# Performance work log

Hardware: AMD Instinct MI355X
Metric: run time of the kernel (lower is better)

Reference implementation:

```python
import jax, jax.numpy as jnp
import numpy as np

B, H = 1, 512
NVAR, NCLS = 16384, 65536
NP, NM = 4096, 4096
NEG = -1e30


def setup_inputs() -> dict:
    key = jax.random.key(0)
    ks = jax.random.split(key, 16)
    s = 0.02  # weight init scale
    return {
        "literal_emb": jax.random.normal(ks[0], (B, 2 * NVAR, H), jnp.float32),
        "clause_emb": jax.random.normal(ks[1], (B, NCLS, H), jnp.float32),
        "pos_idx": jax.random.randint(ks[2], (NP,), 0, NCLS),
        "neg_idx": jax.random.randint(ks[3], (NM,), 0, NCLS),
        "keep_mask": jax.random.randint(ks[4], (NP, NM), 0, 2).astype(bool),
        "taken_mask": jax.random.uniform(ks[5], (NP, NM)) < 0.01,  # sparse exclusion set
        "var_K_w": s * jax.random.normal(ks[6], (H, H), jnp.float32),
        "var_K_b": jnp.zeros((H,), jnp.float32),
        "var_Q_w": s * jax.random.normal(ks[7], (H, H), jnp.float32),
        "var_Q_b": jnp.zeros((H,), jnp.float32),
        "var_attn_w": s * jax.random.normal(ks[8], (1, H), jnp.float32),
        "var_attn_b": jnp.zeros((1,), jnp.float32),
        "W_Q_w": s * jax.random.normal(ks[9], (H, H), jnp.float32),
        "W_Q_b": jnp.zeros((H,), jnp.float32),
        "W_K_w": s * jax.random.normal(ks[10], (H, H), jnp.float32),
        "W_K_b": jnp.zeros((H,), jnp.float32),
    }


def reference(literal_emb, clause_emb, pos_idx, neg_idx, keep_mask, taken_mask,
              var_K_w, var_K_b, var_Q_w, var_Q_b, var_attn_w, var_attn_b,
              W_Q_w, W_Q_b, W_K_w, W_K_b):
    n_vars = literal_emb.shape[1] // 2
    # --- select_var: additive attention over positive literals ---
    K = literal_emb[:, :n_vars]                       # [B, V, H]
    K_t = K @ var_K_w.T + var_K_b                     # [B, V, H]
    Q = clause_emb.sum(axis=1)                        # [B, H] (C_aggr='sum')
    Q_t = Q @ var_Q_w.T + var_Q_b                     # [B, H]
    u = (jnp.tanh(K_t + Q_t[:, None, :]) @ var_attn_w.T + var_attn_b)[..., 0]  # [B, V]
    log_score = jax.nn.log_softmax(u, axis=-1)
    var_logp = jnp.max(log_score, axis=-1)            # [B]
    var_idx = jnp.argmax(log_score, axis=-1)          # [B]
    # --- clause-pair attention over pivot pos/neg clause pools ---
    q = clause_emb[:, pos_idx] @ W_Q_w.T + W_Q_b      # [B, NP, H]
    k = clause_emb[:, neg_idx] @ W_K_w.T + W_K_b      # [B, NM, H]
    h = q.shape[-1]
    scores = jnp.einsum('bnh,bmh->bnm', q, k) / jnp.sqrt(jnp.float32(h))
    # mask_grid_asym: drop invalid (keep_mask==0) and already-taken pairs, log-normalize
    valid = keep_mask & (~taken_mask)                 # [NP, NM]
    masked = jnp.where(valid[None], scores, jnp.float32(NEG))
    flat = masked.reshape(masked.shape[0], -1)        # [B, NP*NM]
    logp = jax.nn.log_softmax(flat, axis=-1)
    C_logp = jnp.max(logp, axis=-1)                   # [B]
    C_flat = jnp.argmax(logp, axis=-1)                # [B]
    M = scores.shape[-1]
    ci, cj = C_flat // M, C_flat % M
    c_idx_pos = pos_idx[ci]                           # map back to global clause ids
    c_idx_neg = neg_idx[cj]
    c_logp = C_logp + var_logp                        # [B]
    return (c_logp, c_idx_pos, c_idx_neg, var_idx)
```

## Files before the change

### kernel.cpp

```cpp
#include <hip/hip_runtime.h>
#include <hip/hip_bf16.h>
#include <math.h>

#define HH 512
#define NVARS 16384
#define NPOS 4096
#define NMS 4096
#define NEGV -1.0e30f
#define RSQRT_H 0.04419417382415922f

typedef unsigned short u16;
typedef __attribute__((ext_vector_type(8))) short bf16x8;
typedef __attribute__((ext_vector_type(4))) float f32x4;

struct SPart { float m; float s; int a; int pad; };

__device__ inline u16 f2bf(float f) {
  unsigned u = __float_as_uint(f);
  unsigned r = (u + 0x7fffu + ((u >> 16) & 1u)) >> 16;
  return (u16)r;
}
__device__ inline float bf2f(u16 h) { return __uint_as_float(((unsigned)h) << 16); }

__device__ inline void wreduce_maxidx(float& v, int& idx) {
#pragma unroll
  for (int m = 1; m < 64; m <<= 1) {
    float ov = __shfl_xor(v, m, 64);
    int oi = __shfl_xor(idx, m, 64);
    if (ov > v || (ov == v && oi < idx)) { v = ov; idx = oi; }
  }
}

__device__ inline float wreduce_sum(float v) {
#pragma unroll
  for (int m = 1; m < 64; m <<= 1) v += __shfl_xor(v, m, 64);
  return v;
}

__device__ __forceinline__ void stage_frag(const u16* src, u16* dst) {
  __builtin_amdgcn_global_load_lds(
      (const __attribute__((address_space(1))) void*)src,
      (__attribute__((address_space(3))) void*)dst, 16, 0, 0);
}

__device__ __forceinline__ void do_tofrag(
    const float* __restrict__ src, u16* __restrict__ hi, u16* __restrict__ lo,
    int frag, int lane) {
  const int R = frag >> 4, K = frag & 15;
  const float* p = src + (size_t)(R * 16 + (lane & 15)) * HH + K * 32 + (lane >> 4) * 8;
  float v[8];
  *(float4*)&v[0] = *(const float4*)p;
  *(float4*)&v[4] = *(const float4*)(p + 4);
  u16 h[8], l[8];
#pragma unroll
  for (int e = 0; e < 8; ++e) { h[e] = f2bf(v[e]); l[e] = f2bf(v[e] - bf2f(h[e])); }
  size_t base = (size_t)frag * 512 + (size_t)lane * 8;
  *(ushort4*)(hi + base) = *(ushort4*)&h[0];
  *(ushort4*)(hi + base + 4) = *(ushort4*)&h[4];
  *(ushort4*)(lo + base) = *(ushort4*)&l[0];
  *(ushort4*)(lo + base + 4) = *(ushort4*)&l[4];
}

__global__ __launch_bounds__(256) void wtofrag_kernel(
    const float* __restrict__ varKw, u16* __restrict__ wkhi, u16* __restrict__ wklo,
    const float* __restrict__ WQw, u16* __restrict__ pwqhi, u16* __restrict__ pwqlo,
    const float* __restrict__ WKw, u16* __restrict__ pwkhi, u16* __restrict__ pwklo) {
  const int wb = blockIdx.x;
  const int m = wb >> 7;
  const int frag = (wb & 127) * 4 + (threadIdx.x >> 6);
  const float* src = (m == 0) ? varKw : (m == 1) ? WQw : WKw;
  u16* hi = (m == 0) ? wkhi : (m == 1) ? pwqhi : pwkhi;
  u16* lo = (m == 0) ? wklo : (m == 1) ? pwqlo : pwklo;
  do_tofrag(src, hi, lo, frag, threadIdx.x & 63);
}

__global__ __launch_bounds__(256) void stream_kernel(
    const float* __restrict__ clause, double* __restrict__ qpart,
    const float* __restrict__ lit, u16* __restrict__ lithi, u16* __restrict__ litlo,
    const void* __restrict__ keep, const void* __restrict__ taken,
    unsigned long long* __restrict__ vmask) {
  const int bid = blockIdx.x;
  const int t = threadIdx.x;
  if (bid < 2048) {
    const int fg = t & 127;
    const int rh = t >> 7;
    const float* base = clause + ((size_t)bid * 32 + rh * 16) * HH + fg * 4;
    float4 v[16];
#pragma unroll
    for (int u = 0; u < 16; ++u)
      v[u] = *(const float4*)(base + (size_t)u * HH);
    double a0 = 0.0, a1 = 0.0, a2 = 0.0, a3 = 0.0;
#pragma unroll
    for (int u = 0; u < 16; ++u) {
      a0 += (double)v[u].x; a1 += (double)v[u].y;
      a2 += (double)v[u].z; a3 += (double)v[u].w;
    }
    double* o = qpart + (size_t)(bid * 2 + rh) * HH + fg * 4;
    o[0] = a0; o[1] = a1; o[2] = a2; o[3] = a3;
  } else if (bid < 6144) {
    const int frag = (bid - 2048) * 4 + (t >> 6);
    do_tofrag(lit, lithi, litlo, frag, t & 63);
  } else {
    __shared__ unsigned half_[256];
    const int pb = bid - 6144;
    const unsigned* kw = (const unsigned*)keep;
    int f = 1;
#pragma unroll
    for (int i = 0; i < 16; ++i) f &= (kw[i] <= 1u);
    const size_t e = (size_t)pb * 8192 + (size_t)t * 32;
    unsigned b = 0;
    if (f) {
      const unsigned* kp = (const unsigned*)keep + e;
      const unsigned* tp = (const unsigned*)taken + e;
      uint4 kv[8], tv[8];
#pragma unroll
      for (int c = 0; c < 8; ++c) { kv[c] = *(const uint4*)(kp + c * 4); }
#pragma unroll
      for (int c = 0; c < 8; ++c) { tv[c] = *(const uint4*)(tp + c * 4); }
#pragma unroll
      for (int c = 0; c < 8; ++c) {
        b |= (unsigned)(kv[c].x && !tv[c].x) << (c * 4 + 0);
        b |= (unsigned)(kv[c].y && !tv[c].y) << (c * 4 + 1);
        b |= (unsigned)(kv[c].z && !tv[c].z) << (c * 4 + 2);
        b |= (unsigned)(kv[c].w && !tv[c].w) << (c * 4 + 3);
      }
    } else {
      const unsigned char* kp = (const unsigned char*)keep + e;
      const unsigned char* tp = (const unsigned char*)taken + e;
      uint4 k0 = *(const uint4*)kp, k1 = *(const uint4*)(kp + 16);
      uint4 t0 = *(const uint4*)tp, t1 = *(const uint4*)(tp + 16);
      unsigned kws[8] = {k0.x, k0.y, k0.z, k0.w, k1.x, k1.y, k1.z, k1.w};
      unsigned tws[8] = {t0.x, t0.y, t0.z, t0.w, t1.x, t1.y, t1.z, t1.w};
#pragma unroll
      for (int c = 0; c < 8; ++c)
#pragma unroll
        for (int y = 0; y < 4; ++y) {
          unsigned kb = (kws[c] >> (8 * y)) & 0xffu;
          unsigned tb = (tws[c] >> (8 * y)) & 0xffu;
          b |= (unsigned)(kb && !tb) << (c * 4 + y);
        }
    }
    half_[t] = b;
    __syncthreads();
    if (t < 128) {
      unsigned long long m = (unsigned long long)half_[t * 2] |
                             ((unsigned long long)half_[t * 2 + 1] << 32);
      vmask[(size_t)pb * 128 + t] = m;
    }
  }
}

__global__ __launch_bounds__(256) void qred_kernel(
    const double* __restrict__ qpart, double* __restrict__ Qd) {
  __shared__ double red[256];
  const int t = threadIdx.x;
  const int h = blockIdx.x * 16 + (t & 15);
  const int chunk = t >> 4;
  double s = 0.0;
  for (int j0 = 0; j0 < 256; j0 += 8) {
    double v[8];
#pragma unroll
    for (int u = 0; u < 8; ++u)
      v[u] = qpart[(size_t)(chunk * 256 + j0 + u) * HH + h];
#pragma unroll
    for (int u = 0; u < 8; ++u) s += v[u];
  }
  red[t] = s;
  __syncthreads();
  for (int off = 8; off > 0; off >>= 1) {
    if (chunk < off) red[t] += red[t + off * 16];
    __syncthreads();
  }
  if (t < 16) Qd[blockIdx.x * 16 + t] = red[t];
}

__global__ __launch_bounds__(256) void prepmv_kernel(
    const double* __restrict__ Qd, const float* __restrict__ varQw,
    const float* __restrict__ varQb, const float* __restrict__ varKb,
    float* __restrict__ tvec) {
  __shared__ double red[256];
  const int t = threadIdx.x;
  const int h = blockIdx.x * 16 + (t & 15);
  const int chunk = t >> 4;
  const float* wrow = varQw + (size_t)h * HH + chunk * 32;
  const double* qd = Qd + chunk * 32;
  double s = 0.0;
  for (int j = 0; j < 32; ++j) s += qd[j] * (double)wrow[j];
  red[t] = s;
  __syncthreads();
  for (int off = 8; off > 0; off >>= 1) {
    if (chunk < off) red[t] += red[t + off * 16];
    __syncthreads();
  }
  if (t < 16) {
    int hh = blockIdx.x * 16 + t;
    tvec[hh] = (float)(red[t] + (double)varQb[hh] + (double)varKb[hh]);
  }
}

#define MFMA16(A, B)                                                                 \
  _Pragma("unroll") for (int i_ = 0; i_ < 4; ++i_)                                   \
  _Pragma("unroll") for (int j_ = 0; j_ < 4; ++j_)                                   \
    acc[i_][j_] = __builtin_amdgcn_mfma_f32_16x16x32_bf16(A[i_], B[j_], acc[i_][j_], 0, 0, 0);

#define MFMAS(AH, AL, BH, BL)                                                        \
  do { MFMA16(AH, BH) MFMA16(AH, BL) MFMA16(AL, BH) } while (0)

__global__ __launch_bounds__(256, 3) void proj_kernel(
    const float* __restrict__ clause,
    const int* __restrict__ pos_idx, const int* __restrict__ neg_idx,
    const u16* __restrict__ pwqhi, const u16* __restrict__ pwqlo,
    const u16* __restrict__ pwkhi, const u16* __restrict__ pwklo,
    const float* __restrict__ bQ, const float* __restrict__ bK,
    u16* __restrict__ qhi, u16* __restrict__ qlo,
    u16* __restrict__ khi, u16* __restrict__ klo) {
  const int* __restrict__ idx = blockIdx.z ? neg_idx : pos_idx;
  const u16* __restrict__ whp = blockIdx.z ? pwkhi : pwqhi;
  const u16* __restrict__ wlp = blockIdx.z ? pwklo : pwqlo;
  const float* __restrict__ bias = blockIdx.z ? bK : bQ;
  u16* __restrict__ ohi = blockIdx.z ? khi : qhi;
  u16* __restrict__ olo = blockIdx.z ? klo : qlo;

  const int t = threadIdx.x, lane = t & 63, wid = t >> 6;
  const int wn = wid & 1, wm = wid >> 1;
  const int row0 = blockIdx.x * 128;
  const int col0 = blockIdx.y * 128;

  const float* bptr[4];
#pragma unroll
  for (int j = 0; j < 4; ++j) {
    int g = idx[row0 + wn * 64 + j * 16 + (lane & 15)];
    bptr[j] = clause + (size_t)g * HH + (lane >> 4) * 8;
  }
  const size_t abase = (size_t)((col0 >> 4) + wm * 4) * 8192 + (size_t)lane * 8;

  f32x4 acc[4][4] = {};
#pragma unroll
  for (int s = 0; s < 16; ++s) {
    float rB[4][8];
    bf16x8 aH[4], aL[4], bH[4], bL[4];
#pragma unroll
    for (int f = 0; f < 4; ++f) {
      *(float4*)&rB[f][0] = *(const float4*)(bptr[f] + s * 32);
      *(float4*)&rB[f][4] = *(const float4*)(bptr[f] + s * 32 + 4);
      size_t oa = abase + (size_t)f * 8192 + (size_t)s * 512;
      aH[f] = *(const bf16x8*)(whp + oa);
      aL[f] = *(const bf16x8*)(wlp + oa);
    }
#pragma unroll
    for (int f = 0; f < 4; ++f)
#pragma unroll
      for (int e = 0; e < 8; ++e) {
        float v = rB[f][e];
        u16 h = f2bf(v);
        bH[f][e] = (short)h;
        bL[f][e] = (short)f2bf(v - bf2f(h));
      }
    MFMA16(aH, bH)
    MFMA16(aL, bH)
    MFMA16(aH, bL)
  }

  const int q4 = lane >> 4;
#pragma unroll
  for (int i = 0; i < 4; ++i) {
    const int hbase = col0 + wm * 64 + i * 16 + q4 * 4;
    float b0 = bias[hbase + 0], b1 = bias[hbase + 1];
    float b2 = bias[hbase + 2], b3 = bias[hbase + 3];
    const int lane16 = (lane & 15) + ((i & 1) * 2 + (q4 >> 1)) * 16;
    const int sub = (q4 & 1) * 4;
#pragma unroll
    for (int j = 0; j < 4; ++j) {
      const int frag = ((row0 + wn * 64 + j * 16) >> 4) * 16 +
                       ((col0 + wm * 64 + i * 16) >> 5);
      size_t base = (size_t)frag * 512 + (size_t)lane16 * 8 + sub;
      ushort4 hv, lv;
      float v;
      v = acc[i][j][0] + b0; hv.x = f2bf(v); lv.x = f2bf(v - bf2f(hv.x));
      v = acc[i][j][1] + b1; hv.y = f2bf(v); lv.y = f2bf(v - bf2f(hv.y));
      v = acc[i][j][2] + b2; hv.z = f2bf(v); lv.z = f2bf(v - bf2f(hv.z));
      v = acc[i][j][3] + b3; hv.w = f2bf(v); lv.w = f2bf(v - bf2f(hv.w));
      *(ushort4*)(ohi + base) = hv;
      *(ushort4*)(olo + base) = lv;
    }
  }
}

__global__ __launch_bounds__(256, 2) void ktu_kernel(
    const u16* __restrict__ lithi, const u16* __restrict__ litlo,
    const u16* __restrict__ wkhi, const u16* __restrict__ wklo,
    const float* __restrict__ tvec, const float* __restrict__ attnw,
    float* __restrict__ upart) {
  __shared__ __align__(16) u16 lds[2][4][8][512];
  const int t = threadIdx.x, lane = t & 63, wid = t >> 6;
  const int wn = wid & 1, wm = wid >> 1;
  const int row0 = blockIdx.x * 128;
  const int l8 = lane * 8;

  const u16* sa = (wid == 0) ? lithi : (wid == 1) ? litlo : (wid == 2) ? wkhi : wklo;
  const int rb = (wid < 2) ? (row0 >> 4) : (blockIdx.y * 8);
  const u16* sab = sa + (size_t)rb * 8192 + l8;

#define KSTAGE(buf, s)                                                        \
  _Pragma("unroll") for (int f_ = 0; f_ < 8; ++f_)                            \
    stage_frag(sab + (size_t)f_ * 8192 + (size_t)(s) * 512,                   \
               &lds[buf][wid][f_][0]);

  KSTAGE(0, 0)
  f32x4 acc[4][4] = {};
#pragma unroll
  for (int s = 0; s < 16; ++s) {
    __syncthreads();
    if (s < 15) { KSTAGE((s + 1) & 1, s + 1) }
    const int b = s & 1;
    bf16x8 aH[4], aL[4], bH[4], bL[4];
#pragma unroll
    for (int f = 0; f < 4; ++f) {
      aH[f] = *(const bf16x8*)&lds[b][0][wn * 4 + f][l8];
      aL[f] = *(const bf16x8*)&lds[b][1][wn * 4 + f][l8];
      bH[f] = *(const bf16x8*)&lds[b][2][wm * 4 + f][l8];
      bL[f] = *(const bf16x8*)&lds[b][3][wm * 4 + f][l8];
    }
    MFMAS(aH, aL, bH, bL);
  }
#undef KSTAGE

  const int cbase = blockIdx.y * 128 + wm * 64;
  float tv[4], aw[4];
#pragma unroll
  for (int j = 0; j < 4; ++j) {
    int c = cbase + j * 16 + (lane & 15);
    tv[j] = tvec[c]; aw[j] = attnw[c];
  }
  float us[4][4];
#pragma unroll
  for (int i = 0; i < 4; ++i)
#pragma unroll
    for (int r = 0; r < 4; ++r) {
      float s = 0.f;
#pragma unroll
      for (int j = 0; j < 4; ++j) {
        float x = acc[i][j][r] + tv[j];
        float th = 1.0f - 2.0f / (__expf(2.0f * x) + 1.0f);
        s += th * aw[j];
      }
      us[i][r] = s;
    }
#pragma unroll
  for (int m = 1; m < 16; m <<= 1)
#pragma unroll
    for (int i = 0; i < 4; ++i)
#pragma unroll
      for (int r = 0; r < 4; ++r) us[i][r] += __shfl_xor(us[i][r], m, 64);
  if ((lane & 15) == 0) {
#pragma unroll
    for (int i = 0; i < 4; ++i)
#pragma unroll
      for (int r = 0; r < 4; ++r) {
        int row = row0 + wn * 64 + i * 16 + (lane >> 4) * 4 + r;
        upart[(size_t)(blockIdx.y * 2 + wm) * NVARS + row] = us[i][r];
      }
  }
}

__global__ __launch_bounds__(256, 2) void scores_kernel(
    const u16* __restrict__ qhi, const u16* __restrict__ qlo,
    const u16* __restrict__ khi, const u16* __restrict__ klo,
    const unsigned long long* __restrict__ vmask, SPart* __restrict__ parts) {
  __shared__ __align__(16) u16 lds[2][4][8][512];
  __shared__ unsigned long long mrow[128][2];
  __shared__ float s_rv[4]; __shared__ int s_ri[4]; __shared__ float s_rs[4];
  __shared__ float s_bm; __shared__ int s_ba;

  const int t = threadIdx.x;
  const int lane = t & 63;
  const int wid = t >> 6;
  const int wn = wid & 1, wm = wid >> 1;
  const int l8 = lane * 8;

  const int bid = blockIdx.x;
  const int xcd = bid & 7, p = bid >> 3;
  const int sp = p >> 6, q = p & 63;
  const int g = xcd * 2 + sp;
  const int bx = (g & 3) * 8 + (q & 7);
  const int by = (g >> 2) * 8 + (q >> 3);

  const int n0 = by * 128;
  const int m0 = bx * 128;

  const u16* sa = (wid == 0) ? qhi : (wid == 1) ? qlo : (wid == 2) ? khi : klo;
  const int rb = (wid < 2) ? (n0 >> 4) : (m0 >> 4);
  const u16* sab = sa + (size_t)rb * 8192 + l8;

#define SSTAGE(buf, s)                                                        \
  _Pragma("unroll") for (int f_ = 0; f_ < 8; ++f_)                            \
    stage_frag(sab + (size_t)f_ * 8192 + (size_t)(s) * 512,                   \
               &lds[buf][wid][f_][0]);

  {
    int r = t >> 1, w = t & 1;
    mrow[r][w] = vmask[(size_t)(n0 + r) * (NMS / 64) + (m0 >> 6) + w];
  }

  SSTAGE(0, 0)
  f32x4 acc[4][4] = {};
#pragma unroll
  for (int s = 0; s < 16; ++s) {
    __syncthreads();
    if (s < 15) { SSTAGE((s + 1) & 1, s + 1) }
    const int b = s & 1;
    bf16x8 aH[4], aL[4], bH[4], bL[4];
#pragma unroll
    for (int f = 0; f < 4; ++f) {
      aH[f] = *(const bf16x8*)&lds[b][0][wn * 4 + f][l8];
      aL[f] = *(const bf16x8*)&lds[b][1][wn * 4 + f][l8];
      bH[f] = *(const bf16x8*)&lds[b][2][wm * 4 + f][l8];
      bL[f] = *(const bf16x8*)&lds[b][3][wm * 4 + f][l8];
    }
    MFMAS(aH, aL, bH, bL);
  }
#undef SSTAGE

  const int rbase = wn * 64 + (lane >> 4) * 4;
  const int cb15 = (lane & 15);

  float mv = NEGV; int mi = 0x7fffffff;
#pragma unroll
  for (int i = 0; i < 4; ++i) {
#pragma unroll
    for (int r = 0; r < 4; ++r) {
      int rl = rbase + i * 16 + r;
      unsigned long long ww = mrow[rl][wm];
      int gb = (n0 + rl) * NMS + m0;
#pragma unroll
      for (int j = 0; j < 4; ++j) {
        int bit = j * 16 + cb15;
        int cl = wm * 64 + bit;
        float sv = acc[i][j][r] * RSQRT_H;
        acc[i][j][r] = sv;
        bool valid = ((ww >> bit) & 1ull) != 0;
        if (valid && (sv > mv || (sv == mv && gb + cl < mi))) { mv = sv; mi = gb + cl; }
      }
    }
  }
  wreduce_maxidx(mv, mi);
  if ((t & 63) == 0) { s_rv[wid] = mv; s_ri[wid] = mi; }
  __syncthreads();
  if (t == 0) {
    float bm = s_rv[0]; int ba = s_ri[0];
    for (int w = 1; w < 4; ++w)
      if (s_rv[w] > bm || (s_rv[w] == bm && s_ri[w] < ba)) { bm = s_rv[w]; ba = s_ri[w]; }
    s_bm = bm; s_ba = ba;
  }
  __syncthreads();
  const float bm = s_bm;

  float se = 0.f;
#pragma unroll
  for (int i = 0; i < 4; ++i) {
#pragma unroll
    for (int r = 0; r < 4; ++r) {
      int rl = rbase + i * 16 + r;
      unsigned long long ww = mrow[rl][wm];
#pragma unroll
      for (int j = 0; j < 4; ++j) {
        int bit = j * 16 + cb15;
        bool valid = ((ww >> bit) & 1ull) != 0;
        if (valid) se += __expf(acc[i][j][r] - bm);
      }
    }
  }
  se = wreduce_sum(se);
  if ((t & 63) == 0) s_rs[wid] = se;
  __syncthreads();
  if (t == 0) {
    SPart pt;
    pt.m = s_bm;
    pt.s = s_rs[0] + s_rs[1] + s_rs[2] + s_rs[3];
    pt.a = s_ba; pt.pad = 0;
    parts[by * 32 + bx] = pt;
  }
}

__global__ __launch_bounds__(256) void usum_kernel(
    const float* __restrict__ upart, SPart* __restrict__ uparts2) {
  __shared__ float s_rv[4]; __shared__ int s_ri[4]; __shared__ float s_rs[4];
  __shared__ float s_bm; __shared__ int s_ba;
  const int t = threadIdx.x;
  const int i = blockIdx.x * 256 + t;
  float u = 0.f;
#pragma unroll
  for (int p = 0; p < 8; ++p) u += upart[(size_t)p * NVARS + i];
  float mv = u; int mi = i;
  wreduce_maxidx(mv, mi);
  if ((t & 63) == 0) { s_rv[t >> 6] = mv; s_ri[t >> 6] = mi; }
  __syncthreads();
  if (t == 0) {
    float bm = s_rv[0]; int ba = s_ri[0];
    for (int w = 1; w < 4; ++w)
      if (s_rv[w] > bm || (s_rv[w] == bm && s_ri[w] < ba)) { bm = s_rv[w]; ba = s_ri[w]; }
    s_bm = bm; s_ba = ba;
  }
  __syncthreads();
  float se = __expf(u - s_bm);
  se = wreduce_sum(se);
  if ((t & 63) == 0) s_rs[t >> 6] = se;
  __syncthreads();
  if (t == 0) {
    SPart p;
    p.m = s_bm;
    p.s = s_rs[0] + s_rs[1] + s_rs[2] + s_rs[3];
    p.a = s_ba; p.pad = 0;
    uparts2[blockIdx.x] = p;
  }
}

__global__ __launch_bounds__(256) void final_kernel(
    const SPart* __restrict__ uparts2, const SPart* __restrict__ parts,
    const int* __restrict__ pos_idx, const int* __restrict__ neg_idx,
    float* __restrict__ out) {
  __shared__ float s_rv[4]; __shared__ int s_ri[4]; __shared__ float s_rs[4];
  __shared__ float s_umax; __shared__ int s_uarg; __shared__ float s_usum;
  __shared__ float s_gm; __shared__ int s_ga;
  const int t = threadIdx.x;

  float mv = -3.0e38f; int mi = 0x7fffffff;
  SPart up;
  if (t < 64) {
    up = uparts2[t];
    mv = up.m; mi = up.a;
  }
  wreduce_maxidx(mv, mi);
  if ((t & 63) == 0) { s_rv[t >> 6] = mv; s_ri[t >> 6] = mi; }
  __syncthreads();
  if (t == 0) {
    float bm = s_rv[0]; int ba = s_ri[0];
    for (int w = 1; w < 4; ++w)
      if (s_rv[w] > bm || (s_rv[w] == bm && s_ri[w] < ba)) { bm = s_rv[w]; ba = s_ri[w]; }
    s_umax = bm; s_uarg = ba;
  }
  __syncthreads();
  float se = (t < 64) ? up.s * __expf(up.m - s_umax) : 0.f;
  se = wreduce_sum(se);
  if ((t & 63) == 0) s_rs[t >> 6] = se;
  __syncthreads();
  if (t == 0) s_usum = s_rs[0] + s_rs[1] + s_rs[2] + s_rs[3];
  __syncthreads();

  mv = NEGV; mi = 0x7fffffff;
  for (int i = t; i < 1024; i += 256) {
    SPart p = parts[i];
    if (p.m > mv || (p.m == mv && p.a < mi)) { mv = p.m; mi = p.a; }
  }
  wreduce_maxidx(mv, mi);
  if ((t & 63) == 0) { s_rv[t >> 6] = mv; s_ri[t >> 6] = mi; }
  __syncthreads();
  if (t == 0) {
    float bm = s_rv[0]; int ba = s_ri[0];
    for (int w = 1; w < 4; ++w)
      if (s_rv[w] > bm || (s_rv[w] == bm && s_ri[w] < ba)) { bm = s_rv[w]; ba = s_ri[w]; }
    s_gm = bm; s_ga = ba;
  }
  __syncthreads();
  const float gm = s_gm;
  float ss = 0.f;
  for (int i = t; i < 1024; i += 256) {
    SPart p = parts[i];
    ss += p.s * __expf(p.m - gm);
  }
  ss = wreduce_sum(ss);
  if ((t & 63) == 0) s_rs[t >> 6] = ss;
  __syncthreads();
  if (t == 0) {
    float gsum = s_rs[0] + s_rs[1] + s_rs[2] + s_rs[3];
    float c_logp = -logf(gsum) - logf(s_usum);
    int ga = s_ga;
    if (ga == 0x7fffffff) ga = 0;
    int ci = ga >> 12, cj = ga & 4095;
    out[0] = c_logp;
    out[1] = (float)pos_idx[ci];
    out[2] = (float)neg_idx[cj];
    out[3] = (float)s_uarg;
  }
}

extern "C" void kernel_launch(void* const* d_in, const int* in_sizes, int n_in,
                              void* d_out, int out_size, void* d_ws, size_t ws_size,
                              hipStream_t stream) {
  (void)in_sizes; (void)n_in; (void)out_size; (void)ws_size;
  const float* lit    = (const float*)d_in[0];
  const float* clause = (const float*)d_in[1];
  const int* pos_idx  = (const int*)d_in[2];
  const int* neg_idx  = (const int*)d_in[3];
  const void* keep    = d_in[4];
  const void* taken   = d_in[5];
  const float* varKw  = (const float*)d_in[6];
  const float* varKb  = (const float*)d_in[7];
  const float* varQw  = (const float*)d_in[8];
  const float* varQb  = (const float*)d_in[9];
  const float* attnw  = (const float*)d_in[10];
  const float* WQw    = (const float*)d_in[12];
  const float* WQb    = (const float*)d_in[13];
  const float* WKw    = (const float*)d_in[14];
  const float* WKb    = (const float*)d_in[15];

  char* ws = (char*)d_ws;
  size_t off = 0;
  auto alloc = [&](size_t b) {
    char* p = ws + off;
    off = (off + b + 255) & ~(size_t)255;
    return p;
  };
  double* qpart              = (double*)alloc((size_t)4096 * HH * 8);
  double* Qd                 = (double*)alloc(HH * 8);
  float* tvec                = (float*)alloc(HH * 4);
  float* upart               = (float*)alloc(8 * (size_t)NVARS * 4);
  unsigned long long* vmask  = (unsigned long long*)alloc((size_t)NPOS * (NMS / 64) * 8);
  u16* qhi                   = (u16*)alloc((size_t)NPOS * HH * 2);
  u16* qlo                   = (u16*)alloc((size_t)NPOS * HH * 2);
  u16* khi                   = (u16*)alloc((size_t)NMS * HH * 2);
  u16* klo                   = (u16*)alloc((size_t)NMS * HH * 2);
  u16* wkhi                  = (u16*)alloc((size_t)HH * HH * 2);
  u16* wklo                  = (u16*)alloc((size_t)HH * HH * 2);
  u16* pwqhi                 = (u16*)alloc((size_t)HH * HH * 2);
  u16* pwqlo                 = (u16*)alloc((size_t)HH * HH * 2);
  u16* pwkhi                 = (u16*)alloc((size_t)HH * HH * 2);
  u16* pwklo                 = (u16*)alloc((size_t)HH * HH * 2);
  u16* lithi                 = (u16*)alloc((size_t)NVARS * HH * 2);
  u16* litlo                 = (u16*)alloc((size_t)NVARS * HH * 2);
  SPart* parts               = (SPart*)alloc(1024 * sizeof(SPart));
  SPart* uparts2             = (SPart*)alloc(64 * sizeof(SPart));

  wtofrag_kernel<<<384, 256, 0, stream>>>(varKw, wkhi, wklo,
                                          WQw, pwqhi, pwqlo,
                                          WKw, pwkhi, pwklo);
  proj_kernel<<<dim3(32, 4, 2), 256, 0, stream>>>(clause, pos_idx, neg_idx,
                                                  pwqhi, pwqlo, pwkhi, pwklo,
                                                  WQb, WKb,
                                                  qhi, qlo, khi, klo);
  stream_kernel<<<8192, 256, 0, stream>>>(clause, qpart, lit, lithi, litlo,
                                          keep, taken, vmask);
  qred_kernel<<<32, 256, 0, stream>>>(qpart, Qd);
  prepmv_kernel<<<32, 256, 0, stream>>>(Qd, varQw, varQb, varKb, tvec);
  scores_kernel<<<1024, 256, 0, stream>>>(qhi, qlo, khi, klo, vmask, parts);
  ktu_kernel<<<dim3(128, 4), 256, 0, stream>>>(lithi, litlo, wkhi, wklo,
                                               tvec, attnw, upart);
  usum_kernel<<<64, 256, 0, stream>>>(upart, uparts2);
  final_kernel<<<1, 256, 0, stream>>>(uparts2, parts, pos_idx, neg_idx,
                                      (float*)d_out);
}
```

Baseline: 246.1 us.

## Fuse literal bf16 split into ktu GEMM and merge weight conversion launch

The ktu GEMM now loads fp32 literal embeddings directly from global memory and splits them into hi/lo bf16 fragments in registers. This removes the separate pass that wrote lithi/litlo (32 MB read, 32 MB written, 32 MB re-read) and drops the LDS staging, using register double-buffering instead. The weight-to-fragment conversion is folded into stream_kernel, which removes one launch. The cost is that each block column (blockIdx.y) re-reads the fp32 literals, so literal reads go up fourfold, and the fragment loads are less coalesced with no LDS reuse.

```diff
diff --git a/kernel.cpp b/kernel.cpp
--- a/kernel.cpp
+++ b/kernel.cpp
@@ -61,24 +61,13 @@
   *(ushort4*)(lo + base + 4) = *(ushort4*)&l[4];
 }
 
-__global__ __launch_bounds__(256) void wtofrag_kernel(
+__global__ __launch_bounds__(256) void stream_kernel(
+    const float* __restrict__ clause, double* __restrict__ qpart,
+    const void* __restrict__ keep, const void* __restrict__ taken,
+    unsigned long long* __restrict__ vmask,
     const float* __restrict__ varKw, u16* __restrict__ wkhi, u16* __restrict__ wklo,
     const float* __restrict__ WQw, u16* __restrict__ pwqhi, u16* __restrict__ pwqlo,
     const float* __restrict__ WKw, u16* __restrict__ pwkhi, u16* __restrict__ pwklo) {
-  const int wb = blockIdx.x;
-  const int m = wb >> 7;
-  const int frag = (wb & 127) * 4 + (threadIdx.x >> 6);
-  const float* src = (m == 0) ? varKw : (m == 1) ? WQw : WKw;
-  u16* hi = (m == 0) ? wkhi : (m == 1) ? pwqhi : pwkhi;
-  u16* lo = (m == 0) ? wklo : (m == 1) ? pwqlo : pwklo;
-  do_tofrag(src, hi, lo, frag, threadIdx.x & 63);
-}
-
-__global__ __launch_bounds__(256) void stream_kernel(
-    const float* __restrict__ clause, double* __restrict__ qpart,
-    const float* __restrict__ lit, u16* __restrict__ lithi, u16* __restrict__ litlo,
-    const void* __restrict__ keep, const void* __restrict__ taken,
-    unsigned long long* __restrict__ vmask) {
   const int bid = blockIdx.x;
   const int t = threadIdx.x;
   if (bid < 2048) {
@@ -97,12 +86,9 @@
     }
     double* o = qpart + (size_t)(bid * 2 + rh) * HH + fg * 4;
     o[0] = a0; o[1] = a1; o[2] = a2; o[3] = a3;
-  } else if (bid < 6144) {
-    const int frag = (bid - 2048) * 4 + (t >> 6);
-    do_tofrag(lit, lithi, litlo, frag, t & 63);
-  } else {
+  } else if (bid < 4096) {
     __shared__ unsigned half_[256];
-    const int pb = bid - 6144;
+    const int pb = bid - 2048;
     const unsigned* kw = (const unsigned*)keep;
     int f = 1;
 #pragma unroll
@@ -147,6 +133,14 @@
                              ((unsigned long long)half_[t * 2 + 1] << 32);
       vmask[(size_t)pb * 128 + t] = m;
     }
+  } else {
+    const int wb = bid - 4096;
+    const int m = wb >> 7;
+    const int frag = (wb & 127) * 4 + (t >> 6);
+    const float* src = (m == 0) ? varKw : (m == 1) ? WQw : WKw;
+    u16* hi = (m == 0) ? wkhi : (m == 1) ? pwqhi : pwkhi;
+    u16* lo = (m == 0) ? wklo : (m == 1) ? pwqlo : pwklo;
+    do_tofrag(src, hi, lo, frag, t & 63);
   }
 }
 
@@ -287,43 +281,62 @@
 }
 
 __global__ __launch_bounds__(256, 2) void ktu_kernel(
-    const u16* __restrict__ lithi, const u16* __restrict__ litlo,
+    const float* __restrict__ lit,
     const u16* __restrict__ wkhi, const u16* __restrict__ wklo,
     const float* __restrict__ tvec, const float* __restrict__ attnw,
     float* __restrict__ upart) {
-  __shared__ __align__(16) u16 lds[2][4][8][512];
   const int t = threadIdx.x, lane = t & 63, wid = t >> 6;
   const int wn = wid & 1, wm = wid >> 1;
   const int row0 = blockIdx.x * 128;
-  const int l8 = lane * 8;
-
-  const u16* sa = (wid == 0) ? lithi : (wid == 1) ? litlo : (wid == 2) ? wkhi : wklo;
-  const int rb = (wid < 2) ? (row0 >> 4) : (blockIdx.y * 8);
-  const u16* sab = sa + (size_t)rb * 8192 + l8;
-
-#define KSTAGE(buf, s)                                                        \
-  _Pragma("unroll") for (int f_ = 0; f_ < 8; ++f_)                            \
-    stage_frag(sab + (size_t)f_ * 8192 + (size_t)(s) * 512,                   \
-               &lds[buf][wid][f_][0]);
-
-  KSTAGE(0, 0)
+  const int arow0 = row0 + wn * 64 + (lane & 15);
+  const int kcol = (lane >> 4) * 8;
+  const size_t bbase = (size_t)(blockIdx.y * 8 + wm * 4) * 8192 + (size_t)lane * 8;
+
+#define KLOADA(s, RAW)                                                               \
+  do {                                                                               \
+    _Pragma("unroll") for (int f_ = 0; f_ < 4; ++f_) {                               \
+      const float* p_ = lit + (size_t)(arow0 + f_ * 16) * HH + (s) * 32 + kcol;      \
+      *(float4*)&RAW[f_][0] = *(const float4*)p_;                                    \
+      *(float4*)&RAW[f_][4] = *(const float4*)(p_ + 4);                              \
+    }                                                                                \
+  } while (0)
+
+#define KLOADB(s, BH, BL)                                                            \
+  do {                                                                               \
+    _Pragma("unroll") for (int f_ = 0; f_ < 4; ++f_) {                               \
+      size_t o_ = bbase + (size_t)f_ * 8192 + (size_t)(s) * 512;                     \
+      BH[f_] = *(const bf16x8*)(wkhi + o_);                                          \
+      BL[f_] = *(const bf16x8*)(wklo + o_);                                          \
+    }                                                                                \
+  } while (0)
+
+#define KCONV(RAW, AH, AL)                                                           \
+  do {                                                                               \
+    _Pragma("unroll") for (int f_ = 0; f_ < 4; ++f_)                                 \
+    _Pragma("unroll") for (int e_ = 0; e_ < 8; ++e_) {                               \
+      float v_ = RAW[f_][e_];                                                        \
+      u16 h_ = f2bf(v_);                                                             \
+      AH[f_][e_] = (short)h_;                                                        \
+      AL[f_][e_] = (short)f2bf(v_ - bf2f(h_));                                       \
+    }                                                                                \
+  } while (0)
+
   f32x4 acc[4][4] = {};
-#pragma unroll
-  for (int s = 0; s < 16; ++s) {
-    __syncthreads();
-    if (s < 15) { KSTAGE((s + 1) & 1, s + 1) }
-    const int b = s & 1;
-    bf16x8 aH[4], aL[4], bH[4], bL[4];
-#pragma unroll
-    for (int f = 0; f < 4; ++f) {
-      aH[f] = *(const bf16x8*)&lds[b][0][wn * 4 + f][l8];
-      aL[f] = *(const bf16x8*)&lds[b][1][wn * 4 + f][l8];
-      bH[f] = *(const bf16x8*)&lds[b][2][wm * 4 + f][l8];
-      bL[f] = *(const bf16x8*)&lds[b][3][wm * 4 + f][l8];
-    }
-    MFMAS(aH, aL, bH, bL);
-  }
-#undef KSTAGE
+  float rA0[4][8], rA1[4][8];
+  bf16x8 fAH[4], fAL[4], bH0[4], bL0[4], bH1[4], bL1[4];
+  KLOADA(0, rA0); KLOADB(0, bH0, bL0);
+#pragma unroll
+  for (int s = 0; s < 16; s += 2) {
+    KLOADA(s + 1, rA1); KLOADB(s + 1, bH1, bL1);
+    KCONV(rA0, fAH, fAL);
+    MFMAS(fAH, fAL, bH0, bL0);
+    if (s + 2 < 16) { KLOADA(s + 2, rA0); KLOADB(s + 2, bH0, bL0); }
+    KCONV(rA1, fAH, fAL);
+    MFMAS(fAH, fAL, bH1, bL1);
+  }
+#undef KLOADA
+#undef KLOADB
+#undef KCONV
 
   const int cbase = blockIdx.y * 128 + wm * 64;
   float tv[4], aw[4];
@@ -626,25 +639,21 @@
   u16* pwqlo                 = (u16*)alloc((size_t)HH * HH * 2);
   u16* pwkhi                 = (u16*)alloc((size_t)HH * HH * 2);
   u16* pwklo                 = (u16*)alloc((size_t)HH * HH * 2);
-  u16* lithi                 = (u16*)alloc((size_t)NVARS * HH * 2);
-  u16* litlo                 = (u16*)alloc((size_t)NVARS * HH * 2);
   SPart* parts               = (SPart*)alloc(1024 * sizeof(SPart));
   SPart* uparts2             = (SPart*)alloc(64 * sizeof(SPart));
 
-  wtofrag_kernel<<<384, 256, 0, stream>>>(varKw, wkhi, wklo,
+  stream_kernel<<<4480, 256, 0, stream>>>(clause, qpart, keep, taken, vmask,
+                                          varKw, wkhi, wklo,
                                           WQw, pwqhi, pwqlo,
                                           WKw, pwkhi, pwklo);
   proj_kernel<<<dim3(32, 4, 2), 256, 0, stream>>>(clause, pos_idx, neg_idx,
                                                   pwqhi, pwqlo, pwkhi, pwklo,
                                                   WQb, WKb,
                                                   qhi, qlo, khi, klo);
-  stream_kernel<<<8192, 256, 0, stream>>>(clause, qpart, lit, lithi, litlo,
-                                          keep, taken, vmask);
   qred_kernel<<<32, 256, 0, stream>>>(qpart, Qd);
   prepmv_kernel<<<32, 256, 0, stream>>>(Qd, varQw, varQb, varKb, tvec);
   scores_kernel<<<1024, 256, 0, stream>>>(qhi, qlo, khi, klo, vmask, parts);
-  ktu_kernel<<<dim3(128, 4), 256, 0, stream>>>(lithi, litlo, wkhi, wklo,
-                                               tvec, attnw, upart);
+  ktu_kernel<<<dim3(128, 4), 256, 0, stream>>>(lit, wkhi, wklo, tvec, attnw, upart);
   usum_kernel<<<64, 256, 0, stream>>>(upart, uparts2);
   final_kernel<<<1, 256, 0, stream>>>(uparts2, parts, pos_idx, neg_idx,
                                       (float*)d_out);
```

Result: no change. 244.5 us (-0.7%).

## Co-schedule mask packing with projection, and scores with streaming work

Applied to the files above, without the earlier changes.

Restructures the launch schedule so two kernels interleave heterogeneous roles by block index. In the first, mask-packing blocks share a launch with the Q/K projection GEMM blocks. In the second, the scores GEMM shares a launch with the clause-sum reduction and the literal hi/lo split. The clause sum now stages rows through LDS with async global-to-LDS loads and produces half as many partials, which shrinks the follow-up reduction. The aim is to overlap memory-bound streaming with MFMA-bound tiles and cut launch count. The risk is that mixed roles and LDS sized for the GEMM lower occupancy for the streaming blocks.

```diff
diff --git a/kernel.cpp b/kernel.cpp
--- a/kernel.cpp
+++ b/kernel.cpp
@@ -38,6 +38,11 @@
 }
 
 __device__ __forceinline__ void stage_frag(const u16* src, u16* dst) {
+  __builtin_amdgcn_global_load_lds(
+      (const __attribute__((address_space(1))) void*)src,
+      (__attribute__((address_space(3))) void*)dst, 16, 0, 0);
+}
+__device__ __forceinline__ void stage_f32(const float* src, float* dst) {
   __builtin_amdgcn_global_load_lds(
       (const __attribute__((address_space(1))) void*)src,
       (__attribute__((address_space(3))) void*)dst, 16, 0, 0);
@@ -60,6 +65,14 @@
   *(ushort4*)(lo + base) = *(ushort4*)&l[0];
   *(ushort4*)(lo + base + 4) = *(ushort4*)&l[4];
 }
+
+#define MFMA16(A, B)                                                                 \
+  _Pragma("unroll") for (int i_ = 0; i_ < 4; ++i_)                                   \
+  _Pragma("unroll") for (int j_ = 0; j_ < 4; ++j_)                                   \
+    acc[i_][j_] = __builtin_amdgcn_mfma_f32_16x16x32_bf16(A[i_], B[j_], acc[i_][j_], 0, 0, 0);
+
+#define MFMAS(AH, AL, BH, BL)                                                        \
+  do { MFMA16(AH, BH) MFMA16(AH, BL) MFMA16(AL, BH) } while (0)
 
 __global__ __launch_bounds__(256) void wtofrag_kernel(
     const float* __restrict__ varKw, u16* __restrict__ wkhi, u16* __restrict__ wklo,
@@ -74,35 +87,21 @@
   do_tofrag(src, hi, lo, frag, threadIdx.x & 63);
 }
 
-__global__ __launch_bounds__(256) void stream_kernel(
-    const float* __restrict__ clause, double* __restrict__ qpart,
-    const float* __restrict__ lit, u16* __restrict__ lithi, u16* __restrict__ litlo,
+__global__ __launch_bounds__(256) void projpack_kernel(
+    const float* __restrict__ clause,
+    const int* __restrict__ pos_idx, const int* __restrict__ neg_idx,
+    const u16* __restrict__ pwqhi, const u16* __restrict__ pwqlo,
+    const u16* __restrict__ pwkhi, const u16* __restrict__ pwklo,
+    const float* __restrict__ bQ, const float* __restrict__ bK,
+    u16* __restrict__ qhi, u16* __restrict__ qlo,
+    u16* __restrict__ khi, u16* __restrict__ klo,
     const void* __restrict__ keep, const void* __restrict__ taken,
     unsigned long long* __restrict__ vmask) {
-  const int bid = blockIdx.x;
+  const int id = blockIdx.x;
   const int t = threadIdx.x;
-  if (bid < 2048) {
-    const int fg = t & 127;
-    const int rh = t >> 7;
-    const float* base = clause + ((size_t)bid * 32 + rh * 16) * HH + fg * 4;
-    float4 v[16];
-#pragma unroll
-    for (int u = 0; u < 16; ++u)
-      v[u] = *(const float4*)(base + (size_t)u * HH);
-    double a0 = 0.0, a1 = 0.0, a2 = 0.0, a3 = 0.0;
-#pragma unroll
-    for (int u = 0; u < 16; ++u) {
-      a0 += (double)v[u].x; a1 += (double)v[u].y;
-      a2 += (double)v[u].z; a3 += (double)v[u].w;
-    }
-    double* o = qpart + (size_t)(bid * 2 + rh) * HH + fg * 4;
-    o[0] = a0; o[1] = a1; o[2] = a2; o[3] = a3;
-  } else if (bid < 6144) {
-    const int frag = (bid - 2048) * 4 + (t >> 6);
-    do_tofrag(lit, lithi, litlo, frag, t & 63);
-  } else {
+  if (id % 9 != 8) {
     __shared__ unsigned half_[256];
-    const int pb = bid - 6144;
+    const int pb = (id / 9) * 8 + (id % 9);
     const unsigned* kw = (const unsigned*)keep;
     int f = 1;
 #pragma unroll
@@ -147,6 +146,251 @@
                              ((unsigned long long)half_[t * 2 + 1] << 32);
       vmask[(size_t)pb * 128 + t] = m;
     }
+    return;
+  }
+  const int pid = id / 9;
+  const int rowt = pid & 31, colt = (pid >> 5) & 3, z = pid >> 7;
+  const int* __restrict__ idx = z ? neg_idx : pos_idx;
+  const u16* __restrict__ whp = z ? pwkhi : pwqhi;
+  const u16* __restrict__ wlp = z ? pwklo : pwqlo;
+  const float* __restrict__ bias = z ? bK : bQ;
+  u16* __restrict__ ohi = z ? khi : qhi;
+  u16* __restrict__ olo = z ? klo : qlo;
+
+  const int lane = t & 63, wid = t >> 6;
+  const int wn = wid & 1, wm = wid >> 1;
+  const int row0 = rowt * 128;
+  const int col0 = colt * 128;
+
+  const float* bptr[4];
+#pragma unroll
+  for (int j = 0; j < 4; ++j) {
+    int g = idx[row0 + wn * 64 + j * 16 + (lane & 15)];
+    bptr[j] = clause + (size_t)g * HH + (lane >> 4) * 8;
+  }
+  const size_t abase = (size_t)((col0 >> 4) + wm * 4) * 8192 + (size_t)lane * 8;
+
+  f32x4 acc[4][4] = {};
+#pragma unroll
+  for (int s = 0; s < 16; ++s) {
+    float rB[4][8];
+    bf16x8 aH[4], aL[4], bH[4], bL[4];
+#pragma unroll
+    for (int f = 0; f < 4; ++f) {
+      *(float4*)&rB[f][0] = *(const float4*)(bptr[f] + s * 32);
+      *(float4*)&rB[f][4] = *(const float4*)(bptr[f] + s * 32 + 4);
+      size_t oa = abase + (size_t)f * 8192 + (size_t)s * 512;
+      aH[f] = *(const bf16x8*)(whp + oa);
+      aL[f] = *(const bf16x8*)(wlp + oa);
+    }
+#pragma unroll
+    for (int f = 0; f < 4; ++f)
+#pragma unroll
+      for (int e = 0; e < 8; ++e) {
+        float v = rB[f][e];
+        u16 h = f2bf(v);
+        bH[f][e] = (short)h;
+        bL[f][e] = (short)f2bf(v - bf2f(h));
+      }
+    MFMA16(aH, bH)
+    MFMA16(aL, bH)
+    MFMA16(aH, bL)
+  }
+
+  const int q4 = lane >> 4;
+#pragma unroll
+  for (int i = 0; i < 4; ++i) {
+    const int hbase = col0 + wm * 64 + i * 16 + q4 * 4;
+    float b0 = bias[hbase + 0], b1 = bias[hbase + 1];
+    float b2 = bias[hbase + 2], b3 = bias[hbase + 3];
+    const int lane16 = (lane & 15) + ((i & 1) * 2 + (q4 >> 1)) * 16;
+    const int sub = (q4 & 1) * 4;
+#pragma unroll
+    for (int j = 0; j < 4; ++j) {
+      const int frag = ((row0 + wn * 64 + j * 16) >> 4) * 16 +
+                       ((col0 + wm * 64 + i * 16) >> 5);
+      size_t base = (size_t)frag * 512 + (size_t)lane16 * 8 + sub;
+      ushort4 hv, lv;
+      float v;
+      v = acc[i][j][0] + b0; hv.x = f2bf(v); lv.x = f2bf(v - bf2f(hv.x));
+      v = acc[i][j][1] + b1; hv.y = f2bf(v); lv.y = f2bf(v - bf2f(hv.y));
+      v = acc[i][j][2] + b2; hv.z = f2bf(v); lv.z = f2bf(v - bf2f(hv.z));
+      v = acc[i][j][3] + b3; hv.w = f2bf(v); lv.w = f2bf(v - bf2f(hv.w));
+      *(ushort4*)(ohi + base) = hv;
+      *(ushort4*)(olo + base) = lv;
+    }
+  }
+}
+
+__global__ __launch_bounds__(256, 2) void mega_kernel(
+    const float* __restrict__ clause, double* __restrict__ qpart,
+    const float* __restrict__ lit, u16* __restrict__ lithi, u16* __restrict__ litlo,
+    const u16* __restrict__ qhi, const u16* __restrict__ qlo,
+    const u16* __restrict__ khi, const u16* __restrict__ klo,
+    const unsigned long long* __restrict__ vmask, SPart* __restrict__ parts) {
+  __shared__ __align__(16) unsigned char smem[67584];
+  __shared__ float s_rv[4]; __shared__ int s_ri[4]; __shared__ float s_rs[4];
+  __shared__ float s_bm; __shared__ int s_ba;
+
+  const int id = blockIdx.x;
+  const int role = id % 6;
+  const int t = threadIdx.x;
+  const int lane = t & 63;
+  const int wid = t >> 6;
+
+  if (role == 1) {
+    const int qb = id / 6;
+    float* fb0 = (float*)smem;
+    float* fb1 = fb0 + 4096;
+    const float* src = clause + (size_t)qb * 64 * HH;
+    const int fg = t & 127, half2 = t >> 7;
+
+#define QSTAGE(BUF, s)                                                        \
+    _Pragma("unroll") for (int c_ = 0; c_ < 4; ++c_) {                        \
+      int j_ = wid * 4 + c_;                                                  \
+      int off_ = (j_ >> 1) * 512 + (j_ & 1) * 256;                            \
+      stage_f32(src + (size_t)(s) * 8 * HH + off_ + lane * 4, (BUF) + off_);  \
+    }
+
+    double a0 = 0.0, a1 = 0.0, a2 = 0.0, a3 = 0.0;
+    QSTAGE(fb0, 0)
+#pragma unroll
+    for (int s = 0; s < 8; ++s) {
+      __syncthreads();
+      float* buf = (s & 1) ? fb1 : fb0;
+      if (s < 7) {
+        float* nbuf = (s & 1) ? fb0 : fb1;
+        QSTAGE(nbuf, s + 1)
+      }
+#pragma unroll
+      for (int r = 0; r < 4; ++r) {
+        float4 v = *(const float4*)&buf[(half2 * 4 + r) * 512 + fg * 4];
+        a0 += (double)v.x; a1 += (double)v.y;
+        a2 += (double)v.z; a3 += (double)v.w;
+      }
+      if (s < 7) __syncthreads();
+    }
+#undef QSTAGE
+    double* o = qpart + (size_t)(qb * 2 + half2) * HH + fg * 4;
+    o[0] = a0; o[1] = a1; o[2] = a2; o[3] = a3;
+    return;
+  }
+  if (role >= 2) {
+    const int li = (id / 6) * 4 + (role - 2);
+    const int frag = li * 4 + wid;
+    do_tofrag(lit, lithi, litlo, frag, lane);
+    return;
+  }
+
+  typedef u16 LdsT[4][8][512];
+  LdsT* lds = (LdsT*)smem;
+  typedef unsigned long long MrowT[2];
+  MrowT* mrow = (MrowT*)(smem + 65536);
+
+  const int wn = wid & 1, wm = wid >> 1;
+  const int l8 = lane * 8;
+
+  const int bid = id / 6;
+  const int xcd = bid & 7, p = bid >> 3;
+  const int sp = p >> 6, q = p & 63;
+  const int g = xcd * 2 + sp;
+  const int bx = (g & 3) * 8 + (q & 7);
+  const int by = (g >> 2) * 8 + (q >> 3);
+
+  const int n0 = by * 128;
+  const int m0 = bx * 128;
+
+  const u16* sa = (wid == 0) ? qhi : (wid == 1) ? qlo : (wid == 2) ? khi : klo;
+  const int rb = (wid < 2) ? (n0 >> 4) : (m0 >> 4);
+  const u16* sab = sa + (size_t)rb * 8192 + l8;
+
+#define SSTAGE(buf, s)                                                        \
+  _Pragma("unroll") for (int f_ = 0; f_ < 8; ++f_)                            \
+    stage_frag(sab + (size_t)f_ * 8192 + (size_t)(s) * 512,                   \
+               &lds[buf][wid][f_][0]);
+
+  {
+    int r = t >> 1, w = t & 1;
+    mrow[r][w] = vmask[(size_t)(n0 + r) * (NMS / 64) + (m0 >> 6) + w];
+  }
+
+  SSTAGE(0, 0)
+  f32x4 acc[4][4] = {};
+#pragma unroll
+  for (int s = 0; s < 16; ++s) {
+    __syncthreads();
+    if (s < 15) { SSTAGE((s + 1) & 1, s + 1) }
+    const int b = s & 1;
+    bf16x8 aH[4], aL[4], bH[4], bL[4];
+#pragma unroll
+    for (int f = 0; f < 4; ++f) {
+      aH[f] = *(const bf16x8*)&lds[b][0][wn * 4 + f][l8];
+      aL[f] = *(const bf16x8*)&lds[b][1][wn * 4 + f][l8];
+      bH[f] = *(const bf16x8*)&lds[b][2][wm * 4 + f][l8];
+      bL[f] = *(const bf16x8*)&lds[b][3][wm * 4 + f][l8];
+    }
+    MFMAS(aH, aL, bH, bL);
+  }
+#undef SSTAGE
+
+  const int rbase = wn * 64 + (lane >> 4) * 4;
+  const int cb15 = (lane & 15);
+
+  float mv = NEGV; int mi = 0x7fffffff;
+#pragma unroll
+  for (int i = 0; i < 4; ++i) {
+#pragma unroll
+    for (int r = 0; r < 4; ++r) {
+      int rl = rbase + i * 16 + r;
+      unsigned long long ww = mrow[rl][wm];
+      int gb = (n0 + rl) * NMS + m0;
+#pragma unroll
+      for (int j = 0; j < 4; ++j) {
+        int bit = j * 16 + cb15;
+        int cl = wm * 64 + bit;
+        float sv = acc[i][j][r] * RSQRT_H;
+        acc[i][j][r] = sv;
+        bool valid = ((ww >> bit) & 1ull) != 0;
+        if (valid && (sv > mv || (sv == mv && gb + cl < mi))) { mv = sv; mi = gb + cl; }
+      }
+    }
+  }
+  wreduce_maxidx(mv, mi);
+  if ((t & 63) == 0) { s_rv[wid] = mv; s_ri[wid] = mi; }
+  __syncthreads();
+  if (t == 0) {
+    float bm = s_rv[0]; int ba = s_ri[0];
+    for (int w = 1; w < 4; ++w)
+      if (s_rv[w] > bm || (s_rv[w] == bm && s_ri[w] < ba)) { bm = s_rv[w]; ba = s_ri[w]; }
+    s_bm = bm; s_ba = ba;
+  }
+  __syncthreads();
+  const float bm = s_bm;
+
+  float se = 0.f;
+#pragma unroll
+  for (int i = 0; i < 4; ++i) {
+#pragma unroll
+    for (int r = 0; r < 4; ++r) {
+      int rl = rbase + i * 16 + r;
+      unsigned long long ww = mrow[rl][wm];
+#pragma unroll
+      for (int j = 0; j < 4; ++j) {
+        int bit = j * 16 + cb15;
+        bool valid = ((ww >> bit) & 1ull) != 0;
+        if (valid) se += __expf(acc[i][j][r] - bm);
+      }
+    }
+  }
+  se = wreduce_sum(se);
+  if ((t & 63) == 0) s_rs[wid] = se;
+  __syncthreads();
+  if (t == 0) {
+    SPart pt;
+    pt.m = s_bm;
+    pt.s = s_rs[0] + s_rs[1] + s_rs[2] + s_rs[3];
+    pt.a = s_ba; pt.pad = 0;
+    parts[by * 32 + bx] = pt;
   }
 }
 
@@ -157,11 +401,11 @@
   const int h = blockIdx.x * 16 + (t & 15);
   const int chunk = t >> 4;
   double s = 0.0;
-  for (int j0 = 0; j0 < 256; j0 += 8) {
+  for (int j0 = 0; j0 < 128; j0 += 8) {
     double v[8];
 #pragma unroll
     for (int u = 0; u < 8; ++u)
-      v[u] = qpart[(size_t)(chunk * 256 + j0 + u) * HH + h];
+      v[u] = qpart[(size_t)(chunk * 128 + j0 + u) * HH + h];
 #pragma unroll
     for (int u = 0; u < 8; ++u) s += v[u];
   }
@@ -198,94 +442,6 @@
   }
 }
 
-#define MFMA16(A, B)                                                                 \
-  _Pragma("unroll") for (int i_ = 0; i_ < 4; ++i_)                                   \
-  _Pragma("unroll") for (int j_ = 0; j_ < 4; ++j_)                                   \
-    acc[i_][j_] = __builtin_amdgcn_mfma_f32_16x16x32_bf16(A[i_], B[j_], acc[i_][j_], 0, 0, 0);
-
-#define MFMAS(AH, AL, BH, BL)                                                        \
-  do { MFMA16(AH, BH) MFMA16(AH, BL) MFMA16(AL, BH) } while (0)
-
-__global__ __launch_bounds__(256, 3) void proj_kernel(
-    const float* __restrict__ clause,
-    const int* __restrict__ pos_idx, const int* __restrict__ neg_idx,
-    const u16* __restrict__ pwqhi, const u16* __restrict__ pwqlo,
-    const u16* __restrict__ pwkhi, const u16* __restrict__ pwklo,
-    const float* __restrict__ bQ, const float* __restrict__ bK,
-    u16* __restrict__ qhi, u16* __restrict__ qlo,
-    u16* __restrict__ khi, u16* __restrict__ klo) {
-  const int* __restrict__ idx = blockIdx.z ? neg_idx : pos_idx;
-  const u16* __restrict__ whp = blockIdx.z ? pwkhi : pwqhi;
-  const u16* __restrict__ wlp = blockIdx.z ? pwklo : pwqlo;
-  const float* __restrict__ bias = blockIdx.z ? bK : bQ;
-  u16* __restrict__ ohi = blockIdx.z ? khi : qhi;
-  u16* __restrict__ olo = blockIdx.z ? klo : qlo;
-
-  const int t = threadIdx.x, lane = t & 63, wid = t >> 6;
-  const int wn = wid & 1, wm = wid >> 1;
-  const int row0 = blockIdx.x * 128;
-  const int col0 = blockIdx.y * 128;
-
-  const float* bptr[4];
-#pragma unroll
-  for (int j = 0; j < 4; ++j) {
-    int g = idx[row0 + wn * 64 + j * 16 + (lane & 15)];
-    bptr[j] = clause + (size_t)g * HH + (lane >> 4) * 8;
-  }
-  const size_t abase = (size_t)((col0 >> 4) + wm * 4) * 8192 + (size_t)lane * 8;
-
-  f32x4 acc[4][4] = {};
-#pragma unroll
-  for (int s = 0; s < 16; ++s) {
-    float rB[4][8];
-    bf16x8 aH[4], aL[4], bH[4], bL[4];
-#pragma unroll
-    for (int f = 0; f < 4; ++f) {
-      *(float4*)&rB[f][0] = *(const float4*)(bptr[f] + s * 32);
-      *(float4*)&rB[f][4] = *(const float4*)(bptr[f] + s * 32 + 4);
-      size_t oa = abase + (size_t)f * 8192 + (size_t)s * 512;
-      aH[f] = *(const bf16x8*)(whp + oa);
-      aL[f] = *(const bf16x8*)(wlp + oa);
-    }
-#pragma unroll
-    for (int f = 0; f < 4; ++f)
-#pragma unroll
-      for (int e = 0; e < 8; ++e) {
-        float v = rB[f][e];
-        u16 h = f2bf(v);
-        bH[f][e] = (short)h;
-        bL[f][e] = (short)f2bf(v - bf2f(h));
-      }
-    MFMA16(aH, bH)
-    MFMA16(aL, bH)
-    MFMA16(aH, bL)
-  }
-
-  const int q4 = lane >> 4;
-#pragma unroll
-  for (int i = 0; i < 4; ++i) {
-    const int hbase = col0 + wm * 64 + i * 16 + q4 * 4;
-    float b0 = bias[hbase + 0], b1 = bias[hbase + 1];
-    float b2 = bias[hbase + 2], b3 = bias[hbase + 3];
-    const int lane16 = (lane & 15) + ((i & 1) * 2 + (q4 >> 1)) * 16;
-    const int sub = (q4 & 1) * 4;
-#pragma unroll
-    for (int j = 0; j < 4; ++j) {
-      const int frag = ((row0 + wn * 64 + j * 16) >> 4) * 16 +
-                       ((col0 + wm * 64 + i * 16) >> 5);
-      size_t base = (size_t)frag * 512 + (size_t)lane16 * 8 + sub;
-      ushort4 hv, lv;
-      float v;
-      v = acc[i][j][0] + b0; hv.x = f2bf(v); lv.x = f2bf(v - bf2f(hv.x));
-      v = acc[i][j][1] + b1; hv.y = f2bf(v); lv.y = f2bf(v - bf2f(hv.y));
-      v = acc[i][j][2] + b2; hv.z = f2bf(v); lv.z = f2bf(v - bf2f(hv.z));
-      v = acc[i][j][3] + b3; hv.w = f2bf(v); lv.w = f2bf(v - bf2f(hv.w));
-      *(ushort4*)(ohi + base) = hv;
-      *(ushort4*)(olo + base) = lv;
-    }
-  }
-}
-
 __global__ __launch_bounds__(256, 2) void ktu_kernel(
     const u16* __restrict__ lithi, const u16* __restrict__ litlo,
     const u16* __restrict__ wkhi, const u16* __restrict__ wklo,
@@ -360,125 +516,6 @@
         int row = row0 + wn * 64 + i * 16 + (lane >> 4) * 4 + r;
         upart[(size_t)(blockIdx.y * 2 + wm) * NVARS + row] = us[i][r];
       }
-  }
-}
-
-__global__ __launch_bounds__(256, 2) void scores_kernel(
-    const u16* __restrict__ qhi, const u16* __restrict__ qlo,
-    const u16* __restrict__ khi, const u16* __restrict__ klo,
-    const unsigned long long* __restrict__ vmask, SPart* __restrict__ parts) {
-  __shared__ __align__(16) u16 lds[2][4][8][512];
-  __shared__ unsigned long long mrow[128][2];
-  __shared__ float s_rv[4]; __shared__ int s_ri[4]; __shared__ float s_rs[4];
-  __shared__ float s_bm; __shared__ int s_ba;
-
-  const int t = threadIdx.x;
-  const int lane = t & 63;
-  const int wid = t >> 6;
-  const int wn = wid & 1, wm = wid >> 1;
-  const int l8 = lane * 8;
-
-  const int bid = blockIdx.x;
-  const int xcd = bid & 7, p = bid >> 3;
-  const int sp = p >> 6, q = p & 63;
-  const int g = xcd * 2 + sp;
-  const int bx = (g & 3) * 8 + (q & 7);
-  const int by = (g >> 2) * 8 + (q >> 3);
-
-  const int n0 = by * 128;
-  const int m0 = bx * 128;
-
-  const u16* sa = (wid == 0) ? qhi : (wid == 1) ? qlo : (wid == 2) ? khi : klo;
-  const int rb = (wid < 2) ? (n0 >> 4) : (m0 >> 4);
-  const u16* sab = sa + (size_t)rb * 8192 + l8;
-
-#define SSTAGE(buf, s)                                                        \
-  _Pragma("unroll") for (int f_ = 0; f_ < 8; ++f_)                            \
-    stage_frag(sab + (size_t)f_ * 8192 + (size_t)(s) * 512,                   \
-               &lds[buf][wid][f_][0]);
-
-  {
-    int r = t >> 1, w = t & 1;
-    mrow[r][w] = vmask[(size_t)(n0 + r) * (NMS / 64) + (m0 >> 6) + w];
-  }
-
-  SSTAGE(0, 0)
-  f32x4 acc[4][4] = {};
-#pragma unroll
-  for (int s = 0; s < 16; ++s) {
-    __syncthreads();
-    if (s < 15) { SSTAGE((s + 1) & 1, s + 1) }
-    const int b = s & 1;
-    bf16x8 aH[4], aL[4], bH[4], bL[4];
-#pragma unroll
-    for (int f = 0; f < 4; ++f) {
-      aH[f] = *(const bf16x8*)&lds[b][0][wn * 4 + f][l8];
-      aL[f] = *(const bf16x8*)&lds[b][1][wn * 4 + f][l8];
-      bH[f] = *(const bf16x8*)&lds[b][2][wm * 4 + f][l8];
-      bL[f] = *(const bf16x8*)&lds[b][3][wm * 4 + f][l8];
-    }
-    MFMAS(aH, aL, bH, bL);
-  }
-#undef SSTAGE
-
-  const int rbase = wn * 64 + (lane >> 4) * 4;
-  const int cb15 = (lane & 15);
-
-  float mv = NEGV; int mi = 0x7fffffff;
-#pragma unroll
-  for (int i = 0; i < 4; ++i) {
-#pragma unroll
-    for (int r = 0; r < 4; ++r) {
-      int rl = rbase + i * 16 + r;
-      unsigned long long ww = mrow[rl][wm];
-      int gb = (n0 + rl) * NMS + m0;
-#pragma unroll
-      for (int j = 0; j < 4; ++j) {
-        int bit = j * 16 + cb15;
-        int cl = wm * 64 + bit;
-        float sv = acc[i][j][r] * RSQRT_H;
-        acc[i][j][r] = sv;
-        bool valid = ((ww >> bit) & 1ull) != 0;
-        if (valid && (sv > mv || (sv == mv && gb + cl < mi))) { mv = sv; mi = gb + cl; }
-      }
-    }
-  }
-  wreduce_maxidx(mv, mi);
-  if ((t & 63) == 0) { s_rv[wid] = mv; s_ri[wid] = mi; }
-  __syncthreads();
-  if (t == 0) {
-    float bm = s_rv[0]; int ba = s_ri[0];
-    for (int w = 1; w < 4; ++w)
-      if (s_rv[w] > bm || (s_rv[w] == bm && s_ri[w] < ba)) { bm = s_rv[w]; ba = s_ri[w]; }
-    s_bm = bm; s_ba = ba;
-  }
-  __syncthreads();
-  const float bm = s_bm;
-
-  float se = 0.f;
-#pragma unroll
-  for (int i = 0; i < 4; ++i) {
-#pragma unroll
-    for (int r = 0; r < 4; ++r) {
-      int rl = rbase + i * 16 + r;
-      unsigned long long ww = mrow[rl][wm];
-#pragma unroll
-      for (int j = 0; j < 4; ++j) {
-        int bit = j * 16 + cb15;
-        bool valid = ((ww >> bit) & 1ull) != 0;
-        if (valid) se += __expf(acc[i][j][r] - bm);
-      }
-    }
-  }
-  se = wreduce_sum(se);
-  if ((t & 63) == 0) s_rs[wid] = se;
-  __syncthreads();
-  if (t == 0) {
-    SPart pt;
-    pt.m = s_bm;
-    pt.s = s_rs[0] + s_rs[1] + s_rs[2] + s_rs[3];
-    pt.a = s_ba; pt.pad = 0;
-    parts[by * 32 + bx] = pt;
   }
 }
 
@@ -611,7 +648,7 @@
     off = (off + b + 255) & ~(size_t)255;
     return p;
   };
-  double* qpart              = (double*)alloc((size_t)4096 * HH * 8);
+  double* qpart              = (double*)alloc((size_t)2048 * HH * 8);
   double* Qd                 = (double*)alloc(HH * 8);
   float* tvec                = (float*)alloc(HH * 4);
   float* upart               = (float*)alloc(8 * (size_t)NVARS * 4);
@@ -634,15 +671,14 @@
   wtofrag_kernel<<<384, 256, 0, stream>>>(varKw, wkhi, wklo,
                                           WQw, pwqhi, pwqlo,
                                           WKw, pwkhi, pwklo);
-  proj_kernel<<<dim3(32, 4, 2), 256, 0, stream>>>(clause, pos_idx, neg_idx,
-                                                  pwqhi, pwqlo, pwkhi, pwklo,
-                                                  WQb, WKb,
-                                                  qhi, qlo, khi, klo);
-  stream_kernel<<<8192, 256, 0, stream>>>(clause, qpart, lit, lithi, litlo,
-                                          keep, taken, vmask);
+  projpack_kernel<<<2304, 256, 0, stream>>>(clause, pos_idx, neg_idx,
+                                            pwqhi, pwqlo, pwkhi, pwklo,
+                                            WQb, WKb, qhi, qlo, khi, klo,
+                                            keep, taken, vmask);
+  mega_kernel<<<6144, 256, 0, stream>>>(clause, qpart, lit, lithi, litlo,
+                                        qhi, qlo, khi, klo, vmask, parts);
   qred_kernel<<<32, 256, 0, stream>>>(qpart, Qd);
   prepmv_kernel<<<32, 256, 0, stream>>>(Qd, varQw, varQb, varKb, tvec);
-  scores_kernel<<<1024, 256, 0, stream>>>(qhi, qlo, khi, klo, vmask, parts);
   ktu_kernel<<<dim3(128, 4), 256, 0, stream>>>(lithi, litlo, wkhi, wklo,
                                                tvec, attnw, upart);
   usum_kernel<<<64, 256, 0, stream>>>(upart, uparts2);
```

Result: slower. 257.9 us (+4.8%).
